# Optimization experiments

Measured on AMD Instinct MI355X. Metric: run time of the kernel, lower is better.

## Reference

```python
import jax, jax.numpy as jnp
import numpy as np

B, T, D, H = 2, 2048, 1024, 16
DH = D // H


def setup_inputs() -> dict:
    key = jax.random.key(0)
    ks = jax.random.split(key, 8)
    s = 1.0 / np.sqrt(D)  # xavier-ish scale
    return {
        "query": jax.random.normal(ks[0], (B, T, D), jnp.float32),
        "key": jax.random.normal(ks[1], (B, T, D), jnp.float32),
        "value": jax.random.normal(ks[2], (B, T, D), jnp.float32),
        "Wq": jax.random.normal(ks[3], (D, D), jnp.float32) * s,
        "bq": jnp.zeros((D,), jnp.float32),
        "Wk": jax.random.normal(ks[4], (D, D), jnp.float32) * s,
        "bk": jnp.zeros((D,), jnp.float32),
        "Wv": jax.random.normal(ks[5], (D, D), jnp.float32) * s,
        "bv": jnp.zeros((D,), jnp.float32),
        "Wo": jax.random.normal(ks[6], (D, D), jnp.float32) * s,
        "bo": jnp.zeros((D,), jnp.float32),
        # causal mask (B, T, T); True = attend
        "mask": jnp.broadcast_to(jnp.tril(jnp.ones((T, T), bool)), (B, T, T)),
    }


def _split_heads(x):  # (B, T, D) -> (B, H, T, Dh)
    return x.reshape(B, T, H, DH).transpose(0, 2, 1, 3)


def reference(query, key, value, Wq, bq, Wk, bk, Wv, bv, Wo, bo, mask):
    q = _split_heads(query @ Wq + bq)
    k = _split_heads(key @ Wk + bk)
    v = _split_heads(value @ Wv + bv)
    scores = jnp.einsum("bhqd,bhkd->bhqk", q, k) / jnp.sqrt(jnp.float32(DH))
    scores = jnp.where(mask[:, None, :, :], scores, -jnp.inf)
    w = jax.nn.softmax(scores, axis=-1)
    out = jnp.einsum("bhqk,bhkd->bhqd", w, v)
    out = out.transpose(0, 2, 1, 3).reshape(B, T, D)  # merge heads
    return out @ Wo + bo
```

## Files before the change

kernel.cpp:

```cpp
#include <hip/hip_runtime.h>

typedef unsigned short u16;
typedef __attribute__((ext_vector_type(4))) float f32x4;
typedef __attribute__((ext_vector_type(8))) short bf16x8;

#define MFMA16(a,b,c) __builtin_amdgcn_mfma_f32_16x16x32_bf16((a),(b),(c),0,0,0)

__device__ inline u16 f2bf(float f){
  union { float f; unsigned u; } v; v.f = f;
  unsigned r = v.u + 0x7FFFu + ((v.u >> 16) & 1u);
  return (u16)(r >> 16);
}
__device__ inline u16 f2bf_fast(float f){
  union { float f; unsigned u; } v; v.f = f;
  return (u16)((v.u + 0x8000u) >> 16);
}
__device__ inline unsigned pk2bf(float x, float y){
  union { float f; unsigned u; } a, b; a.f=x; b.f=y;
  return ((a.u + 0x8000u)>>16) | ((b.u + 0x8000u) & 0xFFFF0000u);
}

typedef const __attribute__((address_space(1))) unsigned int* gas_ptr;
typedef __attribute__((address_space(3))) unsigned int* las_ptr;
__device__ inline void gload_lds16(const u16* g, u16* l){
  __builtin_amdgcn_global_load_lds((gas_ptr)(const void*)g, (las_ptr)(void*)l, 16, 0, 0);
}

struct TwbArgs { const float* W[4]; u16* Wt[4]; };
__global__ void k_twb4(TwbArgs a){
  __shared__ u16 t[32][33];
  const float* W = a.W[blockIdx.z];
  u16* Wt = a.Wt[blockIdx.z];
  int kb = blockIdx.x*32, nb = blockIdx.y*32;
  int tx = threadIdx.x, ty = threadIdx.y;
  #pragma unroll
  for (int i=0;i<32;i+=8)
    t[ty+i][tx] = f2bf(W[(size_t)(kb+ty+i)*1024 + nb+tx]);
  __syncthreads();
  #pragma unroll
  for (int i=0;i<32;i+=8)
    Wt[(size_t)(nb+ty+i)*1024 + kb+tx] = t[tx][ty+i];
}

__global__ void k_tv(const u16* __restrict__ V, u16* __restrict__ VT){
  __shared__ u16 t[32][33];
  int tb = blockIdx.x*32;
  int db = blockIdx.y*32;
  int bh = blockIdx.z;
  int b = bh>>4, h = bh&15;
  int tx = threadIdx.x, ty = threadIdx.y;
  #pragma unroll
  for (int i=0;i<32;i+=8)
    t[ty+i][tx] = V[(size_t)(b*2048 + tb+ty+i)*1024 + h*64 + db+tx];
  __syncthreads();
  #pragma unroll
  for (int i=0;i<32;i+=8)
    VT[(size_t)(bh*64 + db+ty+i)*2048 + tb+tx] = t[tx][ty+i];
}

struct GemmArgs3 { const float* A[3]; const u16* Bt[3]; const float* bias[3]; u16* C[3]; };
__global__ __launch_bounds__(256) void k_gemm3(GemmArgs3 g){
  const int N=1024, K=1024;
  int flat = blockIdx.x + (blockIdx.y<<5) + (blockIdx.z<<8);
  int swz = (flat&7)*96 + (flat>>3);
  int by = swz & 7, bx = (swz>>3) & 31, bz = swz >> 8;
  const float* A = g.A[bz]; const u16* Bt = g.Bt[bz];
  const float* bias = g.bias[bz]; u16* C = g.C[bz];
  __shared__ __attribute__((aligned(16))) float As[128*64];
  __shared__ __attribute__((aligned(16))) u16   Bs[128*64];
  const int tid  = threadIdx.x;
  const int wave = tid>>6, lane = tid&63;
  const int lo = lane&15, hi = lane>>4;
  const int lo7 = lo&7;
  const int row0 = bx*128, col0 = by*128;
  const int wm = (wave>>1)*64, wn = (wave&1)*64;
  f32x4 acc[4][4];
  #pragma unroll
  for (int i=0;i<4;i++)
    #pragma unroll
    for (int j=0;j<4;j++) acc[i][j] = (f32x4){0.f,0.f,0.f,0.f};

  for (int k0=0; k0<K; k0+=64){
    #pragma unroll
    for (int r=0;r<8;r++){
      int ga = r*256 + tid;
      int sr = ga>>4, lg = (ga&15) ^ (sr&7);
      gload_lds16((const u16*)(A + (size_t)(row0+sr)*K + k0 + lg*4), (u16*)(As + ga*4));
    }
    #pragma unroll
    for (int r=0;r<4;r++){
      int c = r*256 + tid;
      int sr = c>>3, lg = (c&7) ^ (sr&7);
      gload_lds16(Bt + (size_t)(col0 + sr)*K + k0 + lg*8, Bs + c*8);
    }
    __syncthreads();
    __builtin_amdgcn_s_setprio(1);
    #pragma unroll
    for (int ks=0;ks<2;ks++){
      bf16x8 af[4], bfr[4];
      #pragma unroll
      for (int mf=0;mf<4;mf++){
        const float* Arow = As + (wm+mf*16+lo)*64;
        int q0 = ks*8 + hi*2;
        f32x4 a0 = *(const f32x4*)(Arow + ((q0  )^lo7)*4);
        f32x4 a1 = *(const f32x4*)(Arow + ((q0+1)^lo7)*4);
        union { unsigned u[4]; bf16x8 v; } pk;
        pk.u[0] = pk2bf(a0[0], a0[1]);
        pk.u[1] = pk2bf(a0[2], a0[3]);
        pk.u[2] = pk2bf(a1[0], a1[1]);
        pk.u[3] = pk2bf(a1[2], a1[3]);
        af[mf] = pk.v;
      }
      #pragma unroll
      for (int nf=0;nf<4;nf++)
        bfr[nf] = *(const bf16x8*)(Bs + (wn+nf*16+lo)*64 + ((ks*4+hi)^lo7)*8);
      #pragma unroll
      for (int mf=0;mf<4;mf++)
        #pragma unroll
        for (int nf=0;nf<4;nf++)
          acc[mf][nf] = MFMA16(af[mf], bfr[nf], acc[mf][nf]);
    }
    __builtin_amdgcn_s_setprio(0);
    __syncthreads();
  }
  #pragma unroll
  for (int mf=0;mf<4;mf++){
    #pragma unroll
    for (int nf=0;nf<4;nf++){
      int r0 = row0 + wm + mf*16 + hi*4;
      int c0 = col0 + wn + nf*16 + lo;
      float bv = bias[c0];
      #pragma unroll
      for (int r=0;r<4;r++)
        C[(size_t)(r0+r)*N + c0] = f2bf(acc[mf][nf][r] + bv);
    }
  }
}

__global__ __launch_bounds__(256) void k_gemmO(const u16* __restrict__ A, const u16* __restrict__ Bt,
                                               const float* __restrict__ bias, float* __restrict__ C){
  const int N=1024, K=1024;
  int f = blockIdx.x;
  int xcd = f & 7, idx = f >> 3;
  int bx = xcd*8 + (idx>>3), by = idx & 7;
  __shared__ __attribute__((aligned(16))) u16 As[64*64];
  __shared__ __attribute__((aligned(16))) u16 Bs[128*64];
  const int tid  = threadIdx.x;
  const int wave = tid>>6, lane = tid&63;
  const int lo = lane&15, hi = lane>>4;
  const int row0 = bx*64, col0 = by*128;
  const int wm = (wave>>1)*32, wn = (wave&1)*64;
  f32x4 acc[2][4];
  #pragma unroll
  for (int i=0;i<2;i++)
    #pragma unroll
    for (int j=0;j<4;j++) acc[i][j] = (f32x4){0.f,0.f,0.f,0.f};

  for (int k0=0; k0<K; k0+=64){
    #pragma unroll
    for (int r=0;r<2;r++){
      int c = r*256 + tid;
      gload_lds16(A + (size_t)(row0 + (c>>3))*K + k0 + (c&7)*8, As + c*8);
    }
    #pragma unroll
    for (int r=0;r<4;r++){
      int c = r*256 + tid;
      gload_lds16(Bt + (size_t)(col0 + (c>>3))*K + k0 + (c&7)*8, Bs + c*8);
    }
    __syncthreads();
    __builtin_amdgcn_s_setprio(1);
    #pragma unroll
    for (int ks=0;ks<2;ks++){
      bf16x8 af[2], bfr[4];
      #pragma unroll
      for (int mf=0;mf<2;mf++)
        af[mf] = *(const bf16x8*)(As + (wm+mf*16+lo)*64 + ks*32 + hi*8);
      #pragma unroll
      for (int nf=0;nf<4;nf++)
        bfr[nf] = *(const bf16x8*)(Bs + (wn+nf*16+lo)*64 + ks*32 + hi*8);
      #pragma unroll
      for (int mf=0;mf<2;mf++)
        #pragma unroll
        for (int nf=0;nf<4;nf++)
          acc[mf][nf] = MFMA16(af[mf], bfr[nf], acc[mf][nf]);
    }
    __builtin_amdgcn_s_setprio(0);
    __syncthreads();
  }
  #pragma unroll
  for (int mf=0;mf<2;mf++){
    #pragma unroll
    for (int nf=0;nf<4;nf++){
      int r0 = row0 + wm + mf*16 + hi*4;
      int c0 = col0 + wn + nf*16 + lo;
      float bv = bias[c0];
      #pragma unroll
      for (int r=0;r<4;r++)
        C[(size_t)(r0+r)*N + c0] = acc[mf][nf][r] + bv;
    }
  }
}

__global__ __launch_bounds__(256) void k_attn(
    const u16* __restrict__ Q, const u16* __restrict__ Kp,
    const u16* __restrict__ VT, u16* __restrict__ O)
{
  const int T=2048, D=1024;
  __shared__ __attribute__((aligned(16))) u16 Ks[2][64*64];
  __shared__ __attribute__((aligned(16))) u16 Vs[2][64*64];
  __shared__ __attribute__((aligned(16))) u16 Plds[4][16*64];
  int f = blockIdx.x + (blockIdx.y<<5);
  int xcd = f & 7, idx = f >> 3;
  const int bh = (xcd<<2) | (idx&3);
  const int qb = 31 - (idx>>2);
  const int b = bh>>4, h = bh&15;
  const int tid = threadIdx.x;
  const int wave = tid>>6, lane = tid&63;
  const int lo = lane&15, hi = lane>>4;
  const int wi = wave>>1, wj = wave&1;
  const int lo7 = lo&7;
  const float NEG = -1e30f;
  const float sc = 0.125f * 1.44269504f;
  const float MC = 64.0f * sc;
  const bf16x8 ones = {0x3F80,0x3F80,0x3F80,0x3F80,0x3F80,0x3F80,0x3F80,0x3F80};

  const int c0 = tid, c1 = 256 + tid;
  const int sr0 = c0>>3, sj0 = (c0&7)^(sr0&7);
  const int sr1 = c1>>3, sj1 = (c1&7)^(sr1&7);
  const u16* Kbase = Kp + (size_t)(b*T)*D + h*64;
  const u16* Vbase = VT + (size_t)(bh*64)*T;
  const size_t kOff0 = (size_t)sr0*D + sj0*8, kOff1 = (size_t)sr1*D + sj1*8;
  const size_t vOff0 = (size_t)sr0*T + sj0*8, vOff1 = (size_t)sr1*T + sj1*8;

  const int qrow0 = qb*64 + wi*32;
  bf16x8 qf[2][2];
  #pragma unroll
  for (int qnf=0;qnf<2;qnf++){
    const u16* Qr = Q + (size_t)(b*T + qrow0 + qnf*16 + lo)*D + h*64;
    qf[qnf][0] = *(const bf16x8*)(Qr + hi*8);
    qf[qnf][1] = *(const bf16x8*)(Qr + 32 + hi*8);
  }

  f32x4 o[2][4];
  #pragma unroll
  for (int i=0;i<2;i++)
    #pragma unroll
    for (int j=0;j<4;j++) o[i][j] = (f32x4){0.f,0.f,0.f,0.f};
  f32x4 lac[2];
  lac[0] = (f32x4){0.f,0.f,0.f,0.f};
  lac[1] = (f32x4){0.f,0.f,0.f,0.f};

  gload_lds16(Kbase + kOff0, &Ks[0][c0*8]);
  gload_lds16(Kbase + kOff1, &Ks[0][c1*8]);
  gload_lds16(Vbase + vOff0, &Vs[0][c0*8]);
  gload_lds16(Vbase + vOff1, &Vs[0][c1*8]);
  __syncthreads();

  u16* Pl = &Plds[wave][0];
  const int kcof0 = ((     hi) ^ lo7)*8;
  const int kcof1 = (( 4 + hi) ^ lo7)*8;
  const int vcof  = ((wj*4+hi) ^ lo7)*8;

  int cur = 0;
  for (int kb=0; kb<=qb; kb++){
    if (kb < qb){
      const u16* Kt = Kbase + (size_t)(kb+1)*64*D;
      const u16* Vt = Vbase + (kb+1)*64;
      gload_lds16(Kt + kOff0, &Ks[cur^1][c0*8]);
      gload_lds16(Kt + kOff1, &Ks[cur^1][c1*8]);
      gload_lds16(Vt + vOff0, &Vs[cur^1][c0*8]);
      gload_lds16(Vt + vOff1, &Vs[cur^1][c1*8]);
    }
    const u16* Kl = Ks[cur];
    const u16* Vl = Vs[cur];
    f32x4 s[2][2];
    __builtin_amdgcn_s_setprio(1);
    #pragma unroll
    for (int knf=0;knf<2;knf++){
      int krow = wj*32 + knf*16 + lo;
      bf16x8 kf0 = *(const bf16x8*)(Kl + krow*64 + kcof0);
      bf16x8 kf1 = *(const bf16x8*)(Kl + krow*64 + kcof1);
      #pragma unroll
      for (int qnf=0;qnf<2;qnf++){
        f32x4 z = (f32x4){0.f,0.f,0.f,0.f};
        z = MFMA16(kf0, qf[qnf][0], z);
        s[knf][qnf] = MFMA16(kf1, qf[qnf][1], z);
      }
    }
    __builtin_amdgcn_s_setprio(0);
    if (kb == qb){
      int ql = wi*32 + lo;
      #pragma unroll
      for (int knf=0;knf<2;knf++){
        int kl0 = wj*32 + knf*16 + 4*hi;
        #pragma unroll
        for (int qnf=0;qnf<2;qnf++){
          int qv = ql + qnf*16;
          #pragma unroll
          for (int r=0;r<4;r++)
            if (kl0 + r > qv) s[knf][qnf][r] = NEG;
        }
      }
    }
    #pragma unroll
    for (int knf=0;knf<2;knf++)
      #pragma unroll
      for (int qnf=0;qnf<2;qnf++){
        float p0 = __builtin_amdgcn_exp2f(__builtin_fmaf(s[knf][qnf][0], sc, -MC));
        float p1 = __builtin_amdgcn_exp2f(__builtin_fmaf(s[knf][qnf][1], sc, -MC));
        float p2 = __builtin_amdgcn_exp2f(__builtin_fmaf(s[knf][qnf][2], sc, -MC));
        float p3 = __builtin_amdgcn_exp2f(__builtin_fmaf(s[knf][qnf][3], sc, -MC));
        unsigned w0 = pk2bf(p0, p1);
        unsigned w1 = pk2bf(p2, p3);
        int gphys = (qnf*4 + knf*2 + (hi>>1)) ^ lo7;
        uint2 wv; wv.x = w0; wv.y = w1;
        *(uint2*)&Pl[lo*64 + gphys*8 + 4*(hi&1)] = wv;
      }
    bf16x8 pa0 = *(const bf16x8*)&Pl[lo*64 + kcof0];
    bf16x8 pa1 = *(const bf16x8*)&Pl[lo*64 + kcof1];
    __builtin_amdgcn_s_setprio(1);
    lac[0] = MFMA16(pa0, ones, lac[0]);
    lac[1] = MFMA16(pa1, ones, lac[1]);
    #pragma unroll
    for (int dhnf=0;dhnf<4;dhnf++){
      bf16x8 vf = *(const bf16x8*)(Vl + (dhnf*16+lo)*64 + vcof);
      o[0][dhnf] = MFMA16(pa0, vf, o[0][dhnf]);
      o[1][dhnf] = MFMA16(pa1, vf, o[1][dhnf]);
    }
    __builtin_amdgcn_s_setprio(0);
    __syncthreads();
    cur ^= 1;
  }
  float* os  = (float*)&Ks[0][0];
  float* lsc = (float*)&Vs[0][0];
  if (wj == 1){
    #pragma unroll
    for (int qnf=0;qnf<2;qnf++){
      #pragma unroll
      for (int dhnf=0;dhnf<4;dhnf++)
        #pragma unroll
        for (int r=0;r<4;r++)
          os[((wi*32 + qnf*16 + 4*hi + r)<<6) + dhnf*16 + lo] = o[qnf][dhnf][r];
      if (lo == 0)
        #pragma unroll
        for (int r=0;r<4;r++)
          lsc[wi*32 + qnf*16 + 4*hi + r] = lac[qnf][r];
    }
  }
  __syncthreads();
  if (wj == 0){
    #pragma unroll
    for (int qnf=0;qnf<2;qnf++)
      #pragma unroll
      for (int r=0;r<4;r++){
        int qloc = wi*32 + qnf*16 + 4*hi + r;
        float lt = lac[qnf][r] + lsc[qloc];
        float rinv = 1.0f / lt;
        #pragma unroll
        for (int dhnf=0;dhnf<4;dhnf++){
          float val = o[qnf][dhnf][r] + os[(qloc<<6) + dhnf*16 + lo];
          O[(size_t)(b*T + qb*64 + qloc)*D + h*64 + dhnf*16 + lo] = f2bf_fast(val * rinv);
        }
      }
  }
}

extern "C" void kernel_launch(void* const* d_in, const int* in_sizes, int n_in,
                              void* d_out, int out_size, void* d_ws, size_t ws_size,
                              hipStream_t stream) {
  const int B=2, T=2048, D=1024;
  const int M = B*T;
  const float* query = (const float*)d_in[0];
  const float* key   = (const float*)d_in[1];
  const float* value = (const float*)d_in[2];
  const float* Wq = (const float*)d_in[3];  const float* bq = (const float*)d_in[4];
  const float* Wk = (const float*)d_in[5];  const float* bk = (const float*)d_in[6];
  const float* Wv = (const float*)d_in[7];  const float* bv = (const float*)d_in[8];
  const float* Wo = (const float*)d_in[9];  const float* bo = (const float*)d_in[10];
  float* out = (float*)d_out;

  char* ws = (char*)d_ws;
  const size_t MB = 1024*1024;
  u16* WqT = (u16*)(ws + 24*MB);
  u16* WkT = (u16*)(ws + 26*MB);
  u16* WvT = (u16*)(ws + 28*MB);
  u16* WoT = (u16*)(ws + 30*MB);
  u16* Qp  = (u16*)(ws + 32*MB);
  u16* Kp  = (u16*)(ws + 40*MB);
  u16* Vp  = (u16*)(ws + 48*MB);
  u16* VTp = (u16*)(ws + 56*MB);
  u16* AO  = (u16*)(ws + 64*MB);

  TwbArgs ta; ta.W[0]=Wq; ta.W[1]=Wk; ta.W[2]=Wv; ta.W[3]=Wo;
  ta.Wt[0]=WqT; ta.Wt[1]=WkT; ta.Wt[2]=WvT; ta.Wt[3]=WoT;
  k_twb4<<<dim3(32,32,4), dim3(32,8), 0, stream>>>(ta);

  GemmArgs3 ga;
  ga.A[0]=query; ga.A[1]=key; ga.A[2]=value;
  ga.Bt[0]=WqT; ga.Bt[1]=WkT; ga.Bt[2]=WvT;
  ga.bias[0]=bq; ga.bias[1]=bk; ga.bias[2]=bv;
  ga.C[0]=Qp; ga.C[1]=Kp; ga.C[2]=Vp;
  k_gemm3<<<dim3(32,8,3), 256, 0, stream>>>(ga);

  k_tv<<<dim3(T/32, 2, 32), dim3(32,8), 0, stream>>>(Vp, VTp);
  k_attn<<<dim3(32,32), 256, 0, stream>>>(Qp, Kp, VTp, AO);
  k_gemmO<<<512, 256, 0, stream>>>(AO, WoT, bo, out);
}
```

Before: 123.5 us.

## Convert A to bf16 at staging and prefetch next tile in registers

The QKV projection GEMM now loads fp32 activations into registers, converts them to bf16 once and stores them to shared memory as bf16. Previously it staged fp32 via async global-to-LDS and each wave converted on every fragment read. The next tile's A load is issued before the MFMA loop so global latency overlaps compute, and the XOR swizzle on the LDS layout is dropped. The conversion is now done once per element, but the change costs extra VGPRs, synchronous global loads, and possible LDS bank conflicts from the unswizzled layout. The weight-transpose kernel launch is also flattened to a 1D grid.

```diff
diff --git a/kernel.cpp b/kernel.cpp
--- a/kernel.cpp
+++ b/kernel.cpp
@@ -27,12 +27,16 @@
 }
 
 struct TwbArgs { const float* W[4]; u16* Wt[4]; };
-__global__ void k_twb4(TwbArgs a){
+__global__ void k_twb(TwbArgs a){
   __shared__ u16 t[32][33];
-  const float* W = a.W[blockIdx.z];
-  u16* Wt = a.Wt[blockIdx.z];
-  int kb = blockIdx.x*32, nb = blockIdx.y*32;
-  int tx = threadIdx.x, ty = threadIdx.y;
+  int w = blockIdx.x;
+  int z = w >> 10;
+  int xy = w & 1023;
+  int kb = (xy & 31)*32, nb = (xy >> 5)*32;
+  const float* W = a.W[z];
+  u16* Wt = a.Wt[z];
+  int tid = threadIdx.x;
+  int tx = tid & 31, ty = tid >> 5;
   #pragma unroll
   for (int i=0;i<32;i+=8)
     t[ty+i][tx] = f2bf(W[(size_t)(kb+ty+i)*1024 + nb+tx]);
@@ -66,12 +70,11 @@
   int by = swz & 7, bx = (swz>>3) & 31, bz = swz >> 8;
   const float* A = g.A[bz]; const u16* Bt = g.Bt[bz];
   const float* bias = g.bias[bz]; u16* C = g.C[bz];
-  __shared__ __attribute__((aligned(16))) float As[128*64];
-  __shared__ __attribute__((aligned(16))) u16   Bs[128*64];
+  __shared__ __attribute__((aligned(16))) u16 As[128*64];
+  __shared__ __attribute__((aligned(16))) u16 Bs[128*64];
   const int tid  = threadIdx.x;
   const int wave = tid>>6, lane = tid&63;
   const int lo = lane&15, hi = lane>>4;
-  const int lo7 = lo&7;
   const int row0 = bx*128, col0 = by*128;
   const int wm = (wave>>1)*64, wn = (wave&1)*64;
   f32x4 acc[4][4];
@@ -80,40 +83,55 @@
     #pragma unroll
     for (int j=0;j<4;j++) acc[i][j] = (f32x4){0.f,0.f,0.f,0.f};
 
+  int arow[4], akof[4];
+  #pragma unroll
+  for (int j=0;j<4;j++){
+    int cj = j*256 + tid;
+    arow[j] = cj>>3; akof[j] = (cj&7)*8;
+  }
+  float4 areg[8];
+
+  #define LOAD_A(k0_) { \
+    _Pragma("unroll") \
+    for (int j=0;j<4;j++){ \
+      const float4* p = (const float4*)(A + (size_t)(row0+arow[j])*K + (k0_) + akof[j]); \
+      areg[2*j]   = p[0]; \
+      areg[2*j+1] = p[1]; \
+    } }
+  #define STORE_A() { \
+    _Pragma("unroll") \
+    for (int j=0;j<4;j++){ \
+      unsigned w0 = pk2bf(areg[2*j].x,   areg[2*j].y); \
+      unsigned w1 = pk2bf(areg[2*j].z,   areg[2*j].w); \
+      unsigned w2 = pk2bf(areg[2*j+1].x, areg[2*j+1].y); \
+      unsigned w3 = pk2bf(areg[2*j+1].z, areg[2*j+1].w); \
+      uint4 wv; wv.x=w0; wv.y=w1; wv.z=w2; wv.w=w3; \
+      *(uint4*)&As[arow[j]*64 + akof[j]] = wv; \
+    } }
+  #define STAGE_B(k0_) { \
+    _Pragma("unroll") \
+    for (int r=0;r<4;r++){ \
+      int c = r*256 + tid; \
+      gload_lds16(Bt + (size_t)(col0 + (c>>3))*K + (k0_) + (c&7)*8, Bs + c*8); \
+    } }
+
+  LOAD_A(0)
+  STAGE_B(0)
+  STORE_A()
+  __syncthreads();
+
   for (int k0=0; k0<K; k0+=64){
-    #pragma unroll
-    for (int r=0;r<8;r++){
-      int ga = r*256 + tid;
-      int sr = ga>>4, lg = (ga&15) ^ (sr&7);
-      gload_lds16((const u16*)(A + (size_t)(row0+sr)*K + k0 + lg*4), (u16*)(As + ga*4));
-    }
-    #pragma unroll
-    for (int r=0;r<4;r++){
-      int c = r*256 + tid;
-      int sr = c>>3, lg = (c&7) ^ (sr&7);
-      gload_lds16(Bt + (size_t)(col0 + sr)*K + k0 + lg*8, Bs + c*8);
-    }
-    __syncthreads();
+    if (k0 + 64 < K) LOAD_A(k0+64)
     __builtin_amdgcn_s_setprio(1);
     #pragma unroll
     for (int ks=0;ks<2;ks++){
       bf16x8 af[4], bfr[4];
       #pragma unroll
-      for (int mf=0;mf<4;mf++){
-        const float* Arow = As + (wm+mf*16+lo)*64;
-        int q0 = ks*8 + hi*2;
-        f32x4 a0 = *(const f32x4*)(Arow + ((q0  )^lo7)*4);
-        f32x4 a1 = *(const f32x4*)(Arow + ((q0+1)^lo7)*4);
-        union { unsigned u[4]; bf16x8 v; } pk;
-        pk.u[0] = pk2bf(a0[0], a0[1]);
-        pk.u[1] = pk2bf(a0[2], a0[3]);
-        pk.u[2] = pk2bf(a1[0], a1[1]);
-        pk.u[3] = pk2bf(a1[2], a1[3]);
-        af[mf] = pk.v;
-      }
+      for (int mf=0;mf<4;mf++)
+        af[mf] = *(const bf16x8*)(As + (wm+mf*16+lo)*64 + ks*32 + hi*8);
       #pragma unroll
       for (int nf=0;nf<4;nf++)
-        bfr[nf] = *(const bf16x8*)(Bs + (wn+nf*16+lo)*64 + ((ks*4+hi)^lo7)*8);
+        bfr[nf] = *(const bf16x8*)(Bs + (wn+nf*16+lo)*64 + ks*32 + hi*8);
       #pragma unroll
       for (int mf=0;mf<4;mf++)
         #pragma unroll
@@ -122,7 +140,13 @@
     }
     __builtin_amdgcn_s_setprio(0);
     __syncthreads();
-  }
+    if (k0 + 64 < K){
+      STORE_A()
+      STAGE_B(k0+64)
+      __syncthreads();
+    }
+  }
+
   #pragma unroll
   for (int mf=0;mf<4;mf++){
     #pragma unroll
@@ -135,6 +159,9 @@
         C[(size_t)(r0+r)*N + c0] = f2bf(acc[mf][nf][r] + bv);
     }
   }
+  #undef LOAD_A
+  #undef STORE_A
+  #undef STAGE_B
 }
 
 __global__ __launch_bounds__(256) void k_gemmO(const u16* __restrict__ A, const u16* __restrict__ Bt,
@@ -369,7 +396,6 @@
                               void* d_out, int out_size, void* d_ws, size_t ws_size,
                               hipStream_t stream) {
   const int B=2, T=2048, D=1024;
-  const int M = B*T;
   const float* query = (const float*)d_in[0];
   const float* key   = (const float*)d_in[1];
   const float* value = (const float*)d_in[2];
@@ -391,9 +417,10 @@
   u16* VTp = (u16*)(ws + 56*MB);
   u16* AO  = (u16*)(ws + 64*MB);
 
-  TwbArgs ta; ta.W[0]=Wq; ta.W[1]=Wk; ta.W[2]=Wv; ta.W[3]=Wo;
+  TwbArgs ta;
+  ta.W[0]=Wq; ta.W[1]=Wk; ta.W[2]=Wv; ta.W[3]=Wo;
   ta.Wt[0]=WqT; ta.Wt[1]=WkT; ta.Wt[2]=WvT; ta.Wt[3]=WoT;
-  k_twb4<<<dim3(32,32,4), dim3(32,8), 0, stream>>>(ta);
+  k_twb<<<4096, 256, 0, stream>>>(ta);
 
   GemmArgs3 ga;
   ga.A[0]=query; ga.A[1]=key; ga.A[2]=value;
```

Result: slower. 164.7 us (+33.4%).
